# Performance work log

Measured on AMD Instinct MI355X. Metric: run time of the kernel, lower is better.

The kernel has to match this reference:

```python
import jax, jax.numpy as jnp
import numpy as np

TOPK = 8
BN_EPS = 1e-5


def setup_inputs() -> dict:
    key = jax.random.key(0)
    ks = jax.random.split(key, 5)
    b, n, d = 2, 1024, 1024
    h, nk, kd = 8, 256, 128  # num_heads, num_keys (sqrt(65536)), key_dims
    ne = nk * nk             # 65536 experts
    scale = 0.02
    return {
        "inputs": jax.random.normal(ks[0], (b, n, d), jnp.float32),
        "gamma": jnp.ones((d,), jnp.float32),
        "beta": jnp.zeros((d,), jnp.float32),
        "w_q": jax.random.normal(ks[1], (2 * h * kd, d), jnp.float32) * scale,
        "keys": jax.random.normal(ks[2], (h, nk, 2, kd), jnp.float32) * scale,
        "key_in": jax.random.normal(ks[3], (ne, d), jnp.float32) * scale,
        "key_out": jax.random.normal(ks[4], (ne, d), jnp.float32) * scale,
    }


def reference(inputs, gamma, beta, w_q, keys, key_in, key_out):
    b, n, d = inputs.shape
    h, nk, _, kd = keys.shape
    k = TOPK

    # BatchNorm1d over flattened tokens (training-mode batch statistics)
    x = inputs.reshape(b * n, d)
    mu = jnp.mean(x, axis=0)
    var = jnp.mean(jnp.square(x - mu), axis=0)  # biased var, as torch BN
    xn = (x - mu) * jax.lax.rsqrt(var + BN_EPS) * gamma + beta

    # query projection -> (2, b, n, h, kd)
    q = (xn @ w_q.T).reshape(b, n, 2, h, kd).transpose(2, 0, 1, 3, 4)

    # similarity with product keys: (2, b, n, h, nk)
    sim = jnp.einsum("pbnhd,hkpd->pbnhk", q, keys)

    # stage 1: per-half top-k
    s, i = jax.lax.top_k(sim, k)          # (2, b, n, h, k)
    sx, sy = s[0], s[1]
    ix, iy = i[0], i[1]

    # stage 2: cartesian combine then top-k of k*k
    all_scores = (sx[..., :, None] + sy[..., None, :]).reshape(b, n, h, k * k)
    all_idx = (ix[..., :, None] * nk + iy[..., None, :]).reshape(b, n, h, k * k)
    scores, pk = jax.lax.top_k(all_scores, k)          # (b, n, h, k)
    idx = jnp.take_along_axis(all_idx, pk, axis=-1)    # (b, n, h, k)

    # gather expert vectors: (b, n, h, k, d)
    w_down = key_in[idx]
    w_up = key_out[idx]

    o = jnp.einsum("bnd,bnhkd->bnhk", inputs, w_down)
    o = jax.nn.gelu(o, approximate=False) * jax.nn.softmax(scores, axis=-1)
    return jnp.einsum("bnhk,bnhkd->bnd", o, w_up)
```

## Files before the change

### kernel.cpp

```cpp
#include <hip/hip_runtime.h>
#include <math.h>

#define TT 2048
#define DD 1024
#define HH 8
#define NKK 256
#define KDD 128
#define TK 8
#define NEE 65536

#define DELTA 2e-5f

#define WS_PS    0
#define WS_PQ    262144
#define WS_A     524288
#define WS_B2    528384
#define WS_FLAG  532480
#define WS_XNH   1048576
#define WS_XNL   5242880
#define WS_Q     9437184
#define WS_SIM   26214400
#define WS_WQH   26214400
#define WS_WQL   30408704
#define WS_IDX   59768832
#define WS_SMW   60293120

typedef short bf16x8 __attribute__((ext_vector_type(8)));
typedef float f32x4 __attribute__((ext_vector_type(4)));

__global__ __launch_bounds__(256) void bn_partial(const float* __restrict__ x,
    double* __restrict__ ps, double* __restrict__ pq)
{
    int col = blockIdx.x * 256 + threadIdx.x;
    int r0 = blockIdx.y * 64;
    double s = 0.0, q = 0.0;
    for (int r = 0; r < 64; ++r) {
        double v = (double)x[(size_t)(r0 + r) * DD + col];
        s += v; q += v * v;
    }
    ps[(size_t)blockIdx.y * DD + col] = s;
    pq[(size_t)blockIdx.y * DD + col] = q;
}

__global__ __launch_bounds__(256) void bn_final(const double* __restrict__ ps,
    const double* __restrict__ pq, const float* __restrict__ gamma,
    const float* __restrict__ beta, float* __restrict__ Aout, float* __restrict__ Bout)
{
    int col = blockIdx.x * 256 + threadIdx.x;
    double s = 0.0, q = 0.0;
    for (int g = 0; g < 32; ++g) { s += ps[(size_t)g * DD + col]; q += pq[(size_t)g * DD + col]; }
    double mu = s / 2048.0;
    double var = q / 2048.0 - mu * mu;
    double rstd = 1.0 / sqrt(var + 1e-5);
    Aout[col] = (float)((double)gamma[col] * rstd);
    Bout[col] = (float)((double)beta[col] - mu * (double)gamma[col] * rstd);
}

__device__ __forceinline__ void split_bf16(float v, unsigned short& h, unsigned short& l)
{
    __bf16 hb = (__bf16)v;
    float hf = (float)hb;
    __bf16 lb = (__bf16)(v - hf);
    h = __builtin_bit_cast(unsigned short, hb);
    l = __builtin_bit_cast(unsigned short, lb);
}

__global__ __launch_bounds__(256) void xn_kernel(const float* __restrict__ x,
    const float* __restrict__ A, const float* __restrict__ B2,
    unsigned short* __restrict__ XNh, unsigned short* __restrict__ XNl)
{
    int i = blockIdx.x * 256 + threadIdx.x;
    float4 v = ((const float4*)x)[i];
    int c = (i & 255) << 2;
    v.x = v.x * A[c + 0] + B2[c + 0];
    v.y = v.y * A[c + 1] + B2[c + 1];
    v.z = v.z * A[c + 2] + B2[c + 2];
    v.w = v.w * A[c + 3] + B2[c + 3];
    ushort4 h, l;
    split_bf16(v.x, h.x, l.x); split_bf16(v.y, h.y, l.y);
    split_bf16(v.z, h.z, l.z); split_bf16(v.w, h.w, l.w);
    ((ushort4*)XNh)[i] = h;
    ((ushort4*)XNl)[i] = l;
}

__global__ __launch_bounds__(256) void wq_convert(const float* __restrict__ wq,
    unsigned short* __restrict__ Wh, unsigned short* __restrict__ Wl)
{
    int i = blockIdx.x * 256 + threadIdx.x;
    float4 v = ((const float4*)wq)[i];
    ushort4 h, l;
    split_bf16(v.x, h.x, l.x); split_bf16(v.y, h.y, l.y);
    split_bf16(v.z, h.z, l.z); split_bf16(v.w, h.w, l.w);
    ((ushort4*)Wh)[i] = h;
    ((ushort4*)Wl)[i] = l;
}

#define LSTR 40
__global__ __launch_bounds__(256) void gemm_q_mfma(
    const unsigned short* __restrict__ Ah, const unsigned short* __restrict__ Al,
    const unsigned short* __restrict__ Bh, const unsigned short* __restrict__ Bl,
    float* __restrict__ C)
{
    __shared__ unsigned short sAh[128 * LSTR], sAl[128 * LSTR];
    __shared__ unsigned short sBh[128 * LSTR], sBl[128 * LSTR];
    int tid = threadIdx.x;
    int lane = tid & 63, w = tid >> 6;
    int wm = w >> 1, wn = w & 1;
    int m0 = blockIdx.x * 128, n0 = blockIdx.y * 128;

    f32x4 acc[4][4];
#pragma unroll
    for (int i = 0; i < 4; ++i)
#pragma unroll
        for (int j = 0; j < 4; ++j)
#pragma unroll
            for (int r = 0; r < 4; ++r) acc[i][j][r] = 0.f;

    int srow = tid >> 1;
    int kc0 = (tid & 1) << 1;
    size_t gA = ((size_t)(m0 + srow) << 10) + (kc0 << 3);
    size_t gB = ((size_t)(n0 + srow) << 10) + (kc0 << 3);
    int ls = srow * LSTR + (kc0 << 3);

    int ao[4], bo[4];
#pragma unroll
    for (int i = 0; i < 4; ++i) {
        ao[i] = (wm * 64 + i * 16 + (lane & 15)) * LSTR + ((lane >> 4) << 3);
        bo[i] = (wn * 64 + i * 16 + (lane & 15)) * LSTR + ((lane >> 4) << 3);
    }

    for (int k0 = 0; k0 < 1024; k0 += 32) {
        float4 vah0 = *(const float4*)(Ah + gA + k0);
        float4 vah1 = *(const float4*)(Ah + gA + k0 + 8);
        float4 val0 = *(const float4*)(Al + gA + k0);
        float4 val1 = *(const float4*)(Al + gA + k0 + 8);
        float4 vbh0 = *(const float4*)(Bh + gB + k0);
        float4 vbh1 = *(const float4*)(Bh + gB + k0 + 8);
        float4 vbl0 = *(const float4*)(Bl + gB + k0);
        float4 vbl1 = *(const float4*)(Bl + gB + k0 + 8);
        *(float4*)(sAh + ls) = vah0;  *(float4*)(sAh + ls + 8) = vah1;
        *(float4*)(sAl + ls) = val0;  *(float4*)(sAl + ls + 8) = val1;
        *(float4*)(sBh + ls) = vbh0;  *(float4*)(sBh + ls + 8) = vbh1;
        *(float4*)(sBl + ls) = vbl0;  *(float4*)(sBl + ls + 8) = vbl1;
        __syncthreads();

        bf16x8 fah[4], fal[4], fbh[4], fbl[4];
#pragma unroll
        for (int i = 0; i < 4; ++i) {
            fah[i] = *(const bf16x8*)(sAh + ao[i]);
            fal[i] = *(const bf16x8*)(sAl + ao[i]);
            fbh[i] = *(const bf16x8*)(sBh + bo[i]);
            fbl[i] = *(const bf16x8*)(sBl + bo[i]);
        }
#pragma unroll
        for (int i = 0; i < 4; ++i)
#pragma unroll
            for (int j = 0; j < 4; ++j) {
                acc[i][j] = __builtin_amdgcn_mfma_f32_16x16x32_bf16(fah[i], fbh[j], acc[i][j], 0, 0, 0);
                acc[i][j] = __builtin_amdgcn_mfma_f32_16x16x32_bf16(fah[i], fbl[j], acc[i][j], 0, 0, 0);
                acc[i][j] = __builtin_amdgcn_mfma_f32_16x16x32_bf16(fal[i], fbh[j], acc[i][j], 0, 0, 0);
            }
        __syncthreads();
    }

    int crow = m0 + wm * 64 + ((lane >> 4) << 2);
    int ccol = n0 + wn * 64 + (lane & 15);
#pragma unroll
    for (int i = 0; i < 4; ++i)
#pragma unroll
        for (int j = 0; j < 4; ++j)
#pragma unroll
            for (int r = 0; r < 4; ++r)
                C[(size_t)(crow + i * 16 + r) * 2048 + ccol + j * 16] = acc[i][j][r];
}

__global__ __launch_bounds__(256) void gemm_nt(
    const float* __restrict__ Abase, const float* __restrict__ Bbase,
    float* __restrict__ Cbase, int lda, int ldb, int ldc, int Kdim, int mode)
{
    const float* A = Abase; const float* B = Bbase; float* C = Cbase;
    if (mode == 1) {
        int z = blockIdx.z;
        int p = z >> 3, h = z & 7;
        A += (size_t)z * 128;
        B += (size_t)h * (NKK * 2 * KDD) + (size_t)p * KDD;
        C += (size_t)p * ((size_t)TT * HH * NKK) + (size_t)h * NKK;
    }
    __shared__ float As[16][132];
    __shared__ float Bs[16][132];
    int tid = threadIdx.x;
    int tx = tid & 15, ty = tid >> 4;
    int m0 = blockIdx.x * 128, n0 = blockIdx.y * 128;
    float acc[8][8];
#pragma unroll
    for (int i = 0; i < 8; ++i)
#pragma unroll
        for (int j = 0; j < 8; ++j) acc[i][j] = 0.f;

    for (int k0 = 0; k0 < Kdim; k0 += 16) {
#pragma unroll
        for (int it = 0; it < 2; ++it) {
            int li = tid + it * 256;
            int row = li >> 2;
            int kc = (li & 3) << 2;
            float4 va = *(const float4*)(A + (size_t)(m0 + row) * lda + k0 + kc);
            As[kc + 0][row] = va.x; As[kc + 1][row] = va.y;
            As[kc + 2][row] = va.z; As[kc + 3][row] = va.w;
            float4 vb = *(const float4*)(B + (size_t)(n0 + row) * ldb + k0 + kc);
            Bs[kc + 0][row] = vb.x; Bs[kc + 1][row] = vb.y;
            Bs[kc + 2][row] = vb.z; Bs[kc + 3][row] = vb.w;
        }
        __syncthreads();
#pragma unroll
        for (int k = 0; k < 16; ++k) {
            float a[8], b[8];
            *(float4*)&a[0] = *(const float4*)&As[k][ty * 4];
            *(float4*)&a[4] = *(const float4*)&As[k][64 + ty * 4];
            *(float4*)&b[0] = *(const float4*)&Bs[k][tx * 4];
            *(float4*)&b[4] = *(const float4*)&Bs[k][64 + tx * 4];
#pragma unroll
            for (int i = 0; i < 8; ++i)
#pragma unroll
                for (int j = 0; j < 8; ++j) acc[i][j] += a[i] * b[j];
        }
        __syncthreads();
    }
#pragma unroll
    for (int i = 0; i < 8; ++i) {
        int m = m0 + ((i < 4) ? (ty * 4 + i) : (64 + ty * 4 + (i - 4)));
        float4 c0 = make_float4(acc[i][0], acc[i][1], acc[i][2], acc[i][3]);
        float4 c1 = make_float4(acc[i][4], acc[i][5], acc[i][6], acc[i][7]);
        *(float4*)(C + (size_t)m * ldc + n0 + tx * 4) = c0;
        *(float4*)(C + (size_t)m * ldc + n0 + 64 + tx * 4) = c1;
    }
}

__device__ __forceinline__ void stage1_half(float v0, float v1, float v2, float v3,
    int lane, int mode, float& keep_v, int& keep_i, float& g7, float& g8)
{
#pragma unroll
    for (int it = 0; it < 9; ++it) {
        float bv = v0; int bj = 0;
        if (v1 > bv) { bv = v1; bj = 1; }
        if (v2 > bv) { bv = v2; bj = 2; }
        if (v3 > bv) { bv = v3; bj = 3; }
        int mi = lane + (bj << 6);
        float mv = bv;
#pragma unroll
        for (int off = 1; off < 64; off <<= 1) {
            float ov = __shfl_xor(mv, off);
            int oi = __shfl_xor(mi, off);
            if (ov > mv || (ov == mv && oi < mi)) { mv = ov; mi = oi; }
        }
        int keeper = (mode == 0) ? (lane >> 3) : (lane & 7);
        if (it < 8 && keeper == it) { keep_v = mv; keep_i = mi; }
        if (it == 7) g7 = mv;
        if (it == 8) g8 = mv;
        if (mi == lane)            v0 = -INFINITY;
        else if (mi == lane + 64)  v1 = -INFINITY;
        else if (mi == lane + 128) v2 = -INFINITY;
        else if (mi == lane + 192) v3 = -INFINITY;
    }
}

__device__ __forceinline__ float stage2_write(float vx, float vy, int vix, int viy,
    int lane, int base, int* __restrict__ IDX, float* __restrict__ SMW)
{
    float mycs = vx + vy;
    int cidx = vix * NKK + viy;
    float s2[9]; int wi2[8];
#pragma unroll
    for (int it = 0; it < 9; ++it) {
        float mv = mycs; int ml = lane;
#pragma unroll
        for (int off = 1; off < 64; off <<= 1) {
            float ov = __shfl_xor(mv, off);
            int ol = __shfl_xor(ml, off);
            if (ov > mv || (ov == mv && ol < ml)) { mv = ov; ml = ol; }
        }
        s2[it] = mv;
        if (it < 8) wi2[it] = __shfl(cidx, ml);
        if (lane == ml) mycs = -INFINITY;
    }
    float e[8]; float esum = 0.f;
#pragma unroll
    for (int it = 0; it < 8; ++it) { e[it] = expf(s2[it] - s2[0]); esum += e[it]; }
    float inv = 1.f / esum;
    if (lane == 0) {
#pragma unroll
        for (int it = 0; it < 8; ++it) { IDX[base + it] = wi2[it]; SMW[base + it] = e[it] * inv; }
    }
    return s2[7] - s2[8];
}

__global__ __launch_bounds__(256) void topk_kernel(
    const float* __restrict__ SIM, int* __restrict__ IDX, float* __restrict__ SMW,
    int* __restrict__ FLAG)
{
    int gw = blockIdx.x * 4 + (threadIdx.x >> 6);
    int lane = threadIdx.x & 63;
    int t = gw >> 3, h = gw & 7;

    float vx = 0.f, vy = 0.f; int vix = 0, viy = 0;
    float g7a, g8a, g7b, g8b;

    const float* s0 = SIM + ((size_t)t * HH + h) * NKK;
    stage1_half(s0[lane], s0[lane + 64], s0[lane + 128], s0[lane + 192],
                lane, 0, vx, vix, g7a, g8a);
    const float* s1 = SIM + (size_t)TT * HH * NKK + ((size_t)t * HH + h) * NKK;
    stage1_half(s1[lane], s1[lane + 64], s1[lane + 128], s1[lane + 192],
                lane, 1, vy, viy, g7b, g8b);

    float gap2 = stage2_write(vx, vy, vix, viy, lane, gw * TK, IDX, SMW);
    if (lane == 0) {
        FLAG[gw] = ((g7a - g8a) < DELTA) | ((g7b - g8b) < DELTA) | (gap2 < DELTA);
    }
}

__global__ __launch_bounds__(64) void fixup_kernel(
    const float* __restrict__ x, const float* __restrict__ Aw,
    const float* __restrict__ B2w, const float* __restrict__ w_q,
    const float* __restrict__ keys, const int* __restrict__ FLAG,
    int* __restrict__ IDX, float* __restrict__ SMW)
{
    int row = blockIdx.x;
    if (!FLAG[row]) return;
    int t = row >> 3, h = row & 7;
    int lane = threadIdx.x;
    __shared__ float xs[DD];
    __shared__ float qs[2][KDD];
    __shared__ float sims[2][NKK];

    for (int c = lane * 4; c < DD; c += 256) {
        float4 v = *(const float4*)(x + (size_t)t * DD + c);
        v.x = v.x * Aw[c + 0] + B2w[c + 0];
        v.y = v.y * Aw[c + 1] + B2w[c + 1];
        v.z = v.z * Aw[c + 2] + B2w[c + 2];
        v.w = v.w * Aw[c + 3] + B2w[c + 3];
        *(float4*)&xs[c] = v;
    }
    __syncthreads();

    for (int p = 0; p < 2; ++p)
        for (int j = 0; j < 2; ++j) {
            int kd = lane + j * 64;
            const float* wr = w_q + ((size_t)((p * HH + h) * KDD) + kd) * DD;
            float acc = 0.f;
            for (int d = 0; d < DD; d += 4) {
                float4 wv = *(const float4*)(wr + d);
                acc += xs[d] * wv.x + xs[d + 1] * wv.y + xs[d + 2] * wv.z + xs[d + 3] * wv.w;
            }
            qs[p][kd] = acc;
        }
    __syncthreads();

    for (int p = 0; p < 2; ++p)
        for (int j = 0; j < 4; ++j) {
            int key = lane + j * 64;
            const float* kr = keys + (((size_t)h * NKK + key) * 2 + p) * KDD;
            float acc = 0.f;
            for (int d = 0; d < KDD; d += 4) {
                float4 kv = *(const float4*)(kr + d);
                acc += qs[p][d] * kv.x + qs[p][d + 1] * kv.y + qs[p][d + 2] * kv.z + qs[p][d + 3] * kv.w;
            }
            sims[p][key] = acc;
        }
    __syncthreads();

    float vx = 0.f, vy = 0.f; int vix = 0, viy = 0;
    float d0, d1, d2, d3;
    stage1_half(sims[0][lane], sims[0][lane + 64], sims[0][lane + 128], sims[0][lane + 192],
                lane, 0, vx, vix, d0, d1);
    stage1_half(sims[1][lane], sims[1][lane + 64], sims[1][lane + 128], sims[1][lane + 192],
                lane, 1, vy, viy, d2, d3);
    stage2_write(vx, vy, vix, viy, lane, row * TK, IDX, SMW);
}

__global__ __launch_bounds__(256) void expert_kernel(
    const float* __restrict__ x, const int* __restrict__ IDX,
    const float* __restrict__ SMW, const float* __restrict__ key_in,
    const float* __restrict__ key_out, float* __restrict__ out)
{
    int t = blockIdx.x;
    int tid = threadIdx.x, lane = tid & 63, w = tid >> 6;
    __shared__ float xs[DD];
    __shared__ float part[4][DD];
    *(float4*)&xs[tid * 4] = *(const float4*)(x + (size_t)t * DD + tid * 4);
    __syncthreads();
    float4 xin[4];
#pragma unroll
    for (int r = 0; r < 4; ++r) xin[r] = *(const float4*)&xs[r * 256 + lane * 4];
    float4 acc[4];
#pragma unroll
    for (int r = 0; r < 4; ++r) acc[r] = make_float4(0.f, 0.f, 0.f, 0.f);

    for (int hh2 = 0; hh2 < 2; ++hh2) {
        int hh = w * 2 + hh2;
        for (int k = 0; k < TK; ++k) {
            int base = (t * HH + hh) * TK + k;
            int e = IDX[base];
            float wt = SMW[base];
            const float* ki = key_in + (size_t)e * DD;
            const float* ko = key_out + (size_t)e * DD;
            float4 kin[4], kout[4];
#pragma unroll
            for (int r = 0; r < 4; ++r) kin[r] = *(const float4*)(ki + r * 256 + lane * 4);
#pragma unroll
            for (int r = 0; r < 4; ++r) kout[r] = *(const float4*)(ko + r * 256 + lane * 4);
            float p = 0.f;
#pragma unroll
            for (int r = 0; r < 4; ++r)
                p += xin[r].x * kin[r].x + xin[r].y * kin[r].y
                   + xin[r].z * kin[r].z + xin[r].w * kin[r].w;
#pragma unroll
            for (int off = 1; off < 64; off <<= 1) p += __shfl_xor(p, off);
            float g = 0.5f * p * (1.f + erff(p * 0.70710678118654752440f));
            float go = g * wt;
#pragma unroll
            for (int r = 0; r < 4; ++r) {
                acc[r].x += go * kout[r].x; acc[r].y += go * kout[r].y;
                acc[r].z += go * kout[r].z; acc[r].w += go * kout[r].w;
            }
        }
    }
#pragma unroll
    for (int r = 0; r < 4; ++r) *(float4*)&part[w][r * 256 + lane * 4] = acc[r];
    __syncthreads();
    int c = tid * 4;
    float4 s0 = *(const float4*)&part[0][c];
    float4 s1 = *(const float4*)&part[1][c];
    float4 s2 = *(const float4*)&part[2][c];
    float4 s3 = *(const float4*)&part[3][c];
    float4 o;
    o.x = (s0.x + s1.x) + (s2.x + s3.x);
    o.y = (s0.y + s1.y) + (s2.y + s3.y);
    o.z = (s0.z + s1.z) + (s2.z + s3.z);
    o.w = (s0.w + s1.w) + (s2.w + s3.w);
    *(float4*)(out + (size_t)t * DD + c) = o;
}

extern "C" void kernel_launch(void* const* d_in, const int* in_sizes, int n_in,
                              void* d_out, int out_size, void* d_ws, size_t ws_size,
                              hipStream_t stream)
{
    const float* x       = (const float*)d_in[0];
    const float* gamma   = (const float*)d_in[1];
    const float* beta    = (const float*)d_in[2];
    const float* w_q     = (const float*)d_in[3];
    const float* keys    = (const float*)d_in[4];
    const float* key_in  = (const float*)d_in[5];
    const float* key_out = (const float*)d_in[6];
    float* out = (float*)d_out;
    char* ws = (char*)d_ws;

    double* ps  = (double*)(ws + WS_PS);
    double* pq  = (double*)(ws + WS_PQ);
    float*  Aw  = (float*)(ws + WS_A);
    float*  B2w = (float*)(ws + WS_B2);
    int*    FLAGw = (int*)(ws + WS_FLAG);
    unsigned short* XNh = (unsigned short*)(ws + WS_XNH);
    unsigned short* XNl = (unsigned short*)(ws + WS_XNL);
    unsigned short* WQh = (unsigned short*)(ws + WS_WQH);
    unsigned short* WQl = (unsigned short*)(ws + WS_WQL);
    float*  Q   = (float*)(ws + WS_Q);
    float*  SIMw= (float*)(ws + WS_SIM);
    int*    IDXw= (int*)(ws + WS_IDX);
    float*  SMWw= (float*)(ws + WS_SMW);

    bn_partial<<<dim3(4, 32), 256, 0, stream>>>(x, ps, pq);
    bn_final<<<4, 256, 0, stream>>>(ps, pq, gamma, beta, Aw, B2w);
    xn_kernel<<<2048, 256, 0, stream>>>(x, Aw, B2w, XNh, XNl);
    wq_convert<<<2048, 256, 0, stream>>>(w_q, WQh, WQl);
    gemm_q_mfma<<<dim3(16, 16), 256, 0, stream>>>(XNh, XNl, WQh, WQl, Q);
    gemm_nt<<<dim3(16, 2, 16), 256, 0, stream>>>(Q, keys, SIMw, 2048, 256, 2048, 128, 1);
    topk_kernel<<<4096, 256, 0, stream>>>(SIMw, IDXw, SMWw, FLAGw);
    fixup_kernel<<<16384, 64, 0, stream>>>(x, Aw, B2w, w_q, keys, FLAGw, IDXw, SMWw);
    expert_kernel<<<2048, 256, 0, stream>>>(x, IDXw, SMWw, key_in, key_out, out);
}
```

Before: 443.6 us.

## Split-K the query GEMM, software-pipeline expert gathers, widen fixup delta

The query projection GEMM now uses 128x64 tiles and a two-way split over K, writing two partial outputs that a new qadd kernel sums. This raises the block count from 256 to 1024 so more of the GPU is busy. The expert kernel stages indices and weights in shared memory, double-buffers key_in/key_out row loads with nontemporal loads, and fully unrolls the 16 experts per wave to hide gather latency. DELTA grows from 2e-5 to 1e-4, which likely sends more near-tie rows to the exact fixup path and costs extra work there. The split-K path also adds an extra pass over Q.

```diff
diff --git a/kernel.cpp b/kernel.cpp
--- a/kernel.cpp
+++ b/kernel.cpp
@@ -9,7 +9,7 @@
 #define TK 8
 #define NEE 65536
 
-#define DELTA 2e-5f
+#define DELTA 1e-4f
 
 #define WS_PS    0
 #define WS_PQ    262144
@@ -22,11 +22,13 @@
 #define WS_SIM   26214400
 #define WS_WQH   26214400
 #define WS_WQL   30408704
+#define WS_QP1   42991616
 #define WS_IDX   59768832
 #define WS_SMW   60293120
 
 typedef short bf16x8 __attribute__((ext_vector_type(8)));
 typedef float f32x4 __attribute__((ext_vector_type(4)));
+typedef float fvec4 __attribute__((ext_vector_type(4)));
 
 __global__ __launch_bounds__(256) void bn_partial(const float* __restrict__ x,
     double* __restrict__ ps, double* __restrict__ pq)
@@ -99,63 +101,67 @@
 __global__ __launch_bounds__(256) void gemm_q_mfma(
     const unsigned short* __restrict__ Ah, const unsigned short* __restrict__ Al,
     const unsigned short* __restrict__ Bh, const unsigned short* __restrict__ Bl,
-    float* __restrict__ C)
+    float* __restrict__ C0, float* __restrict__ C1)
 {
     __shared__ unsigned short sAh[128 * LSTR], sAl[128 * LSTR];
-    __shared__ unsigned short sBh[128 * LSTR], sBl[128 * LSTR];
-    int tid = threadIdx.x;
-    int lane = tid & 63, w = tid >> 6;
+    __shared__ unsigned short sBh[64 * LSTR],  sBl[64 * LSTR];
+    int tid = threadIdx.x, lane = tid & 63, w = tid >> 6;
     int wm = w >> 1, wn = w & 1;
-    int m0 = blockIdx.x * 128, n0 = blockIdx.y * 128;
-
-    f32x4 acc[4][4];
+    int m0 = blockIdx.x * 128, n0 = blockIdx.y * 64;
+    int kbase = blockIdx.z * 512;
+    float* C = blockIdx.z ? C1 : C0;
+
+    f32x4 acc[4][2];
 #pragma unroll
     for (int i = 0; i < 4; ++i)
 #pragma unroll
-        for (int j = 0; j < 4; ++j)
+        for (int j = 0; j < 2; ++j)
 #pragma unroll
             for (int r = 0; r < 4; ++r) acc[i][j][r] = 0.f;
 
-    int srow = tid >> 1;
-    int kc0 = (tid & 1) << 1;
-    size_t gA = ((size_t)(m0 + srow) << 10) + (kc0 << 3);
-    size_t gB = ((size_t)(n0 + srow) << 10) + (kc0 << 3);
-    int ls = srow * LSTR + (kc0 << 3);
-
-    int ao[4], bo[4];
-#pragma unroll
-    for (int i = 0; i < 4; ++i) {
+    int arow = tid >> 1, ahalf = tid & 1;
+    size_t gA = (size_t)(m0 + arow) * 1024 + kbase + ahalf * 16;
+    int lsA = arow * LSTR + ahalf * 16;
+    int brow = tid >> 2, bq = tid & 3;
+    size_t gB = (size_t)(n0 + brow) * 1024 + kbase + bq * 8;
+    int lsB = brow * LSTR + bq * 8;
+
+    int ao[4], bo[2];
+#pragma unroll
+    for (int i = 0; i < 4; ++i)
         ao[i] = (wm * 64 + i * 16 + (lane & 15)) * LSTR + ((lane >> 4) << 3);
-        bo[i] = (wn * 64 + i * 16 + (lane & 15)) * LSTR + ((lane >> 4) << 3);
-    }
-
-    for (int k0 = 0; k0 < 1024; k0 += 32) {
-        float4 vah0 = *(const float4*)(Ah + gA + k0);
-        float4 vah1 = *(const float4*)(Ah + gA + k0 + 8);
-        float4 val0 = *(const float4*)(Al + gA + k0);
-        float4 val1 = *(const float4*)(Al + gA + k0 + 8);
-        float4 vbh0 = *(const float4*)(Bh + gB + k0);
-        float4 vbh1 = *(const float4*)(Bh + gB + k0 + 8);
-        float4 vbl0 = *(const float4*)(Bl + gB + k0);
-        float4 vbl1 = *(const float4*)(Bl + gB + k0 + 8);
-        *(float4*)(sAh + ls) = vah0;  *(float4*)(sAh + ls + 8) = vah1;
-        *(float4*)(sAl + ls) = val0;  *(float4*)(sAl + ls + 8) = val1;
-        *(float4*)(sBh + ls) = vbh0;  *(float4*)(sBh + ls + 8) = vbh1;
-        *(float4*)(sBl + ls) = vbl0;  *(float4*)(sBl + ls + 8) = vbl1;
+#pragma unroll
+    for (int j = 0; j < 2; ++j)
+        bo[j] = (wn * 32 + j * 16 + (lane & 15)) * LSTR + ((lane >> 4) << 3);
+
+    for (int k0 = 0; k0 < 512; k0 += 32) {
+        float4 ah0 = *(const float4*)(Ah + gA + k0);
+        float4 ah1 = *(const float4*)(Ah + gA + k0 + 8);
+        float4 al0 = *(const float4*)(Al + gA + k0);
+        float4 al1 = *(const float4*)(Al + gA + k0 + 8);
+        float4 bh0 = *(const float4*)(Bh + gB + k0);
+        float4 bl0 = *(const float4*)(Bl + gB + k0);
+        *(float4*)(sAh + lsA) = ah0;  *(float4*)(sAh + lsA + 8) = ah1;
+        *(float4*)(sAl + lsA) = al0;  *(float4*)(sAl + lsA + 8) = al1;
+        *(float4*)(sBh + lsB) = bh0;
+        *(float4*)(sBl + lsB) = bl0;
         __syncthreads();
 
-        bf16x8 fah[4], fal[4], fbh[4], fbl[4];
+        bf16x8 fah[4], fal[4], fbh[2], fbl[2];
 #pragma unroll
         for (int i = 0; i < 4; ++i) {
             fah[i] = *(const bf16x8*)(sAh + ao[i]);
             fal[i] = *(const bf16x8*)(sAl + ao[i]);
-            fbh[i] = *(const bf16x8*)(sBh + bo[i]);
-            fbl[i] = *(const bf16x8*)(sBl + bo[i]);
+        }
+#pragma unroll
+        for (int j = 0; j < 2; ++j) {
+            fbh[j] = *(const bf16x8*)(sBh + bo[j]);
+            fbl[j] = *(const bf16x8*)(sBl + bo[j]);
         }
 #pragma unroll
         for (int i = 0; i < 4; ++i)
 #pragma unroll
-            for (int j = 0; j < 4; ++j) {
+            for (int j = 0; j < 2; ++j) {
                 acc[i][j] = __builtin_amdgcn_mfma_f32_16x16x32_bf16(fah[i], fbh[j], acc[i][j], 0, 0, 0);
                 acc[i][j] = __builtin_amdgcn_mfma_f32_16x16x32_bf16(fah[i], fbl[j], acc[i][j], 0, 0, 0);
                 acc[i][j] = __builtin_amdgcn_mfma_f32_16x16x32_bf16(fal[i], fbh[j], acc[i][j], 0, 0, 0);
@@ -164,14 +170,24 @@
     }
 
     int crow = m0 + wm * 64 + ((lane >> 4) << 2);
-    int ccol = n0 + wn * 64 + (lane & 15);
+    int ccol = n0 + wn * 32 + (lane & 15);
 #pragma unroll
     for (int i = 0; i < 4; ++i)
 #pragma unroll
-        for (int j = 0; j < 4; ++j)
+        for (int j = 0; j < 2; ++j)
 #pragma unroll
             for (int r = 0; r < 4; ++r)
                 C[(size_t)(crow + i * 16 + r) * 2048 + ccol + j * 16] = acc[i][j][r];
+}
+
+__global__ __launch_bounds__(256) void qadd_kernel(float* __restrict__ Q,
+    const float* __restrict__ P1)
+{
+    int i = blockIdx.x * 256 + threadIdx.x;
+    float4 a = ((const float4*)Q)[i];
+    float4 b = ((const float4*)P1)[i];
+    a.x += b.x; a.y += b.y; a.z += b.z; a.w += b.w;
+    ((float4*)Q)[i] = a;
 }
 
 __global__ __launch_bounds__(256) void gemm_nt(
@@ -376,6 +392,30 @@
     stage2_write(vx, vy, vix, viy, lane, row * TK, IDX, SMW);
 }
 
+__device__ __forceinline__ fvec4 ntload4(const float* p)
+{
+    return __builtin_nontemporal_load((const fvec4*)p);
+}
+
+#define PRELOAD(KIN, KOUT, K)  do {                                          \
+    const float* ki_ = key_in  + (size_t)es[eb + (K)] * DD + lane * 4;       \
+    const float* ko_ = key_out + (size_t)es[eb + (K)] * DD + lane * 4;       \
+    _Pragma("unroll") for (int r = 0; r < 4; ++r) {                          \
+        KIN[r]  = ntload4(ki_ + r * 256);                                    \
+        KOUT[r] = ntload4(ko_ + r * 256); } } while (0)
+
+#define BODY(KIN, KOUT, K) do {                                              \
+    float p_ = 0.f;                                                          \
+    _Pragma("unroll") for (int r = 0; r < 4; ++r)                            \
+        p_ += KIN[r].x * xin[r].x + KIN[r].y * xin[r].y                      \
+            + KIN[r].z * xin[r].z + KIN[r].w * xin[r].w;                     \
+    _Pragma("unroll") for (int off = 1; off < 64; off <<= 1)                 \
+        p_ += __shfl_xor(p_, off);                                           \
+    float g_ = 0.5f * p_ * (1.f + erff(p_ * 0.70710678118654752440f));       \
+    float go_ = g_ * sw[eb + (K)];                                           \
+    _Pragma("unroll") for (int r = 0; r < 4; ++r)                            \
+        acc[r] += go_ * KOUT[r]; } while (0)
+
 __global__ __launch_bounds__(256) void expert_kernel(
     const float* __restrict__ x, const int* __restrict__ IDX,
     const float* __restrict__ SMW, const float* __restrict__ key_in,
@@ -383,60 +423,40 @@
 {
     int t = blockIdx.x;
     int tid = threadIdx.x, lane = tid & 63, w = tid >> 6;
-    __shared__ float xs[DD];
     __shared__ float part[4][DD];
-    *(float4*)&xs[tid * 4] = *(const float4*)(x + (size_t)t * DD + tid * 4);
+    __shared__ int   es[64];
+    __shared__ float sw[64];
+    if (tid < 64) { es[tid] = IDX[t * 64 + tid]; sw[tid] = SMW[t * 64 + tid]; }
+    fvec4 xin[4];
+#pragma unroll
+    for (int r = 0; r < 4; ++r)
+        xin[r] = *(const fvec4*)(x + (size_t)t * DD + r * 256 + lane * 4);
+    fvec4 acc[4];
+#pragma unroll
+    for (int r = 0; r < 4; ++r) acc[r] = (fvec4){0.f, 0.f, 0.f, 0.f};
     __syncthreads();
-    float4 xin[4];
-#pragma unroll
-    for (int r = 0; r < 4; ++r) xin[r] = *(const float4*)&xs[r * 256 + lane * 4];
-    float4 acc[4];
-#pragma unroll
-    for (int r = 0; r < 4; ++r) acc[r] = make_float4(0.f, 0.f, 0.f, 0.f);
-
-    for (int hh2 = 0; hh2 < 2; ++hh2) {
-        int hh = w * 2 + hh2;
-        for (int k = 0; k < TK; ++k) {
-            int base = (t * HH + hh) * TK + k;
-            int e = IDX[base];
-            float wt = SMW[base];
-            const float* ki = key_in + (size_t)e * DD;
-            const float* ko = key_out + (size_t)e * DD;
-            float4 kin[4], kout[4];
-#pragma unroll
-            for (int r = 0; r < 4; ++r) kin[r] = *(const float4*)(ki + r * 256 + lane * 4);
-#pragma unroll
-            for (int r = 0; r < 4; ++r) kout[r] = *(const float4*)(ko + r * 256 + lane * 4);
-            float p = 0.f;
-#pragma unroll
-            for (int r = 0; r < 4; ++r)
-                p += xin[r].x * kin[r].x + xin[r].y * kin[r].y
-                   + xin[r].z * kin[r].z + xin[r].w * kin[r].w;
-#pragma unroll
-            for (int off = 1; off < 64; off <<= 1) p += __shfl_xor(p, off);
-            float g = 0.5f * p * (1.f + erff(p * 0.70710678118654752440f));
-            float go = g * wt;
-#pragma unroll
-            for (int r = 0; r < 4; ++r) {
-                acc[r].x += go * kout[r].x; acc[r].y += go * kout[r].y;
-                acc[r].z += go * kout[r].z; acc[r].w += go * kout[r].w;
-            }
-        }
-    }
-#pragma unroll
-    for (int r = 0; r < 4; ++r) *(float4*)&part[w][r * 256 + lane * 4] = acc[r];
+
+    int eb = w * 16;
+    fvec4 kinA[4], koutA[4], kinB[4], koutB[4];
+    PRELOAD(kinA, koutA, 0);
+#pragma unroll
+    for (int k = 0; k < 16; k += 2) {
+        PRELOAD(kinB, koutB, k + 1);
+        BODY(kinA, koutA, k);
+        if (k + 2 < 16) PRELOAD(kinA, koutA, k + 2);
+        BODY(kinB, koutB, k + 1);
+    }
+
+#pragma unroll
+    for (int r = 0; r < 4; ++r) *(fvec4*)&part[w][r * 256 + lane * 4] = acc[r];
     __syncthreads();
     int c = tid * 4;
-    float4 s0 = *(const float4*)&part[0][c];
-    float4 s1 = *(const float4*)&part[1][c];
-    float4 s2 = *(const float4*)&part[2][c];
-    float4 s3 = *(const float4*)&part[3][c];
-    float4 o;
-    o.x = (s0.x + s1.x) + (s2.x + s3.x);
-    o.y = (s0.y + s1.y) + (s2.y + s3.y);
-    o.z = (s0.z + s1.z) + (s2.z + s3.z);
-    o.w = (s0.w + s1.w) + (s2.w + s3.w);
-    *(float4*)(out + (size_t)t * DD + c) = o;
+    fvec4 s0 = *(const fvec4*)&part[0][c];
+    fvec4 s1 = *(const fvec4*)&part[1][c];
+    fvec4 s2 = *(const fvec4*)&part[2][c];
+    fvec4 s3 = *(const fvec4*)&part[3][c];
+    fvec4 o = (s0 + s1) + (s2 + s3);
+    *(fvec4*)(out + (size_t)t * DD + c) = o;
 }
 
 extern "C" void kernel_launch(void* const* d_in, const int* in_sizes, int n_in,
@@ -463,6 +483,7 @@
     unsigned short* WQh = (unsigned short*)(ws + WS_WQH);
     unsigned short* WQl = (unsigned short*)(ws + WS_WQL);
     float*  Q   = (float*)(ws + WS_Q);
+    float*  QP1 = (float*)(ws + WS_QP1);
     float*  SIMw= (float*)(ws + WS_SIM);
     int*    IDXw= (int*)(ws + WS_IDX);
     float*  SMWw= (float*)(ws + WS_SMW);
@@ -471,7 +492,8 @@
     bn_final<<<4, 256, 0, stream>>>(ps, pq, gamma, beta, Aw, B2w);
     xn_kernel<<<2048, 256, 0, stream>>>(x, Aw, B2w, XNh, XNl);
     wq_convert<<<2048, 256, 0, stream>>>(w_q, WQh, WQl);
-    gemm_q_mfma<<<dim3(16, 16), 256, 0, stream>>>(XNh, XNl, WQh, WQl, Q);
+    gemm_q_mfma<<<dim3(16, 32, 2), 256, 0, stream>>>(XNh, XNl, WQh, WQl, Q, QP1);
+    qadd_kernel<<<4096, 256, 0, stream>>>(Q, QP1);
     gemm_nt<<<dim3(16, 2, 16), 256, 0, stream>>>(Q, keys, SIMw, 2048, 256, 2048, 128, 1);
     topk_kernel<<<4096, 256, 0, stream>>>(SIMw, IDXw, SMWw, FLAGw);
     fixup_kernel<<<16384, 64, 0, stream>>>(x, Aw, B2w, w_q, keys, FLAGw, IDXw, SMWw);
```

Measured after the change: 492.6 us. +11.0%, slower.
